# Kernel optimization log

Hardware: AMD Instinct MI355X
Metric: run time of the kernel (lower is better)

The kernel has to match this reference:

```python
import jax, jax.numpy as jnp
import numpy as np

B, IN, OUT, K, RES, WDIM = 8, 512, 512, 3, 64, 512
CONV_RC = 1.0 / np.sqrt(K * K * IN).astype(np.float32)   # gain*lrmul/sqrt(fan_in), gain=lrmul=1
DENSE_RC = 1.0 / np.sqrt(WDIM).astype(np.float32)
CONV_INIT_STD = float(CONV_RC)   # init_std = he_std / lrmul
DENSE_INIT_STD = float(DENSE_RC)


def setup_inputs() -> dict:
    key = jax.random.key(0)
    k1, k2, k3, k4 = jax.random.split(key, 4)
    return {
        "x": jax.random.normal(k1, (B, IN, RES, RES), jnp.float32),
        "y": jax.random.normal(k2, (B, WDIM), jnp.float32),
        "w": jax.random.normal(k3, (K, K, IN, OUT), jnp.float32) * CONV_INIT_STD,
        "w_mod": jax.random.normal(k4, (WDIM, IN), jnp.float32) * DENSE_INIT_STD,
        "b_mod": jnp.zeros((IN,), jnp.float32),
    }


def reference(x, y, w, w_mod, b_mod):
    # equalized-lr runtime scaling
    w_s = w * CONV_RC                                   # [K,K,IN,OUT]
    # style: s = dense(y) + bias + 1
    s = y @ (w_mod * DENSE_RC) + b_mod + 1.0            # [B,IN]
    # modulate per-sample weights
    ww = w_s[None] * s[:, None, None, :, None]          # [B,K,K,IN,OUT]
    # demodulate
    d = jax.lax.rsqrt(jnp.sum(jnp.square(ww), axis=(1, 2, 3)) + 1e-8)  # [B,OUT]
    ww = ww * d[:, None, None, None, :]
    # fused modconv: grouped conv with groups = B
    xr = x.reshape(1, B * IN, RES, RES)
    wk = jnp.transpose(ww, (1, 2, 3, 0, 4)).reshape(K, K, IN, B * OUT)
    out = jax.lax.conv_general_dilated(
        xr, wk, window_strides=(1, 1), padding="SAME",
        dimension_numbers=("NCHW", "HWIO", "NCHW"),
        feature_group_count=B)
    return out.reshape(B, OUT, RES, RES)
```

## Files before the change

kernel.cpp:

```cpp
#include <hip/hip_runtime.h>
#include <hip/hip_bf16.h>

typedef __bf16 bf16x8 __attribute__((ext_vector_type(8)));
typedef float f32x16 __attribute__((ext_vector_type(16)));
typedef unsigned short u16;
typedef u16 u16x8 __attribute__((ext_vector_type(8)));

#define DENSE_RC 0.0441941738f
#define CONV_RC  0.0147313913f

__device__ inline u16 f2bf(float v) {
  union { float f; unsigned u; } x; x.f = v;
  unsigned r = x.u + 0x7fffu + ((x.u >> 16) & 1u);
  return (u16)(r >> 16);
}

__device__ inline void gload16(const void* g, void* l) {
  __builtin_amdgcn_global_load_lds(
      (const __attribute__((address_space(1))) unsigned int*)g,
      (__attribute__((address_space(3))) unsigned int*)l, 16, 0, 0);
}

__global__ void style_k(const float* __restrict__ y, const float* __restrict__ wm,
                        const float* __restrict__ bm, float* __restrict__ s) {
  const int tid = threadIdx.x, lane = tid & 63, wv = tid >> 6;
  const int idx = blockIdx.x * 64 + lane;
  const int b = idx >> 9, i = idx & 511;
  const float* yb = y + b * 512;
  float acc = 0.f;
  const int j0 = wv * 128;
#pragma unroll 8
  for (int j = j0; j < j0 + 128; ++j) acc += yb[j] * wm[j * 512 + i];
  __shared__ float red[4][64];
  red[wv][lane] = acc;
  __syncthreads();
  if (wv == 0) {
    float a = red[0][lane] + red[1][lane] + red[2][lane] + red[3][lane];
    s[idx] = a * DENSE_RC + bm[i] + 1.0f;
  }
}

__global__ void wsq_k(const float* __restrict__ w, float* __restrict__ wsq) {
  const int idx = blockIdx.x * 256 + threadIdx.x;
  float a = 0.f;
#pragma unroll
  for (int t = 0; t < 9; ++t) { float v = w[(size_t)t * 262144 + idx]; a += v * v; }
  wsq[idx] = a;
}

__global__ void demod_k(const float* __restrict__ s, const float* __restrict__ wsq,
                        float* __restrict__ dmd) {
  const int tid = threadIdx.x, lane = tid & 63, wv = tid >> 6;
  const int idx = blockIdx.x * 64 + lane;
  const int b = idx >> 9, o = idx & 511;
  const float* sb = s + b * 512;
  float a = 0.f;
  const int i0 = wv * 128;
#pragma unroll 4
  for (int i = i0; i < i0 + 128; ++i) { float sv = sb[i]; a += sv * sv * wsq[i * 512 + o]; }
  __shared__ float red[4][64];
  red[wv][lane] = a;
  __syncthreads();
  if (wv == 0) {
    float t = red[0][lane] + red[1][lane] + red[2][lane] + red[3][lane];
    dmd[idx] = rsqrtf(t * (CONV_RC * CONV_RC) + 1e-8f);
  }
}

__global__ void modw_k(const float* __restrict__ w, const float* __restrict__ s,
                       const float* __restrict__ dmd, u16* __restrict__ wwb) {
  const int blk = blockIdx.x;
  const int ob = blk & 7, ib = (blk >> 3) & 15, t = blk >> 7;
  __shared__ float lw[32][65];
  const int tid = threadIdx.x;
#pragma unroll
  for (int k = 0; k < 8; ++k) {
    const int e = tid + k * 256;
    const int i = e >> 6, o = e & 63;
    lw[i][o] = w[(size_t)t * 262144 + (size_t)(ib * 32 + i) * 512 + ob * 64 + o];
  }
  __syncthreads();
  const int oo = tid >> 2, q = tid & 3;
  const int ii0 = q * 8;
  for (int b = 0; b < 8; ++b) {
    const float f = CONV_RC * dmd[b * 512 + ob * 64 + oo];
    u16x8 pk;
#pragma unroll
    for (int j = 0; j < 8; ++j)
      pk[j] = f2bf(lw[ii0 + j][oo] * s[b * 512 + ib * 32 + ii0 + j] * f);
    *(u16x8*)(wwb + ((size_t)(b * 9 + t) * 512 + ob * 64 + oo) * 512 + ib * 32 + ii0) = pk;
  }
}

__global__ void border_k(u16* __restrict__ xpad) {
  const int idx = blockIdx.x * 256 + threadIdx.x;
  const int chunk = idx & 63;
  const int p = (idx >> 6) % 260;
  const int b = idx / (260 * 64);
  int row, col;
  if (p < 66)       { row = 0;       col = p; }
  else if (p < 132) { row = 65;      col = p - 66; }
  else if (p < 196) { row = p - 131; col = 0; }
  else              { row = p - 195; col = 65; }
  u16x8 z = {0, 0, 0, 0, 0, 0, 0, 0};
  *(u16x8*)(xpad + ((size_t)(b * 66 + row) * 66 + col) * 512 + chunk * 8) = z;
}

__global__ void fill_k(const float* __restrict__ x, u16* __restrict__ xpad) {
  const int blk = blockIdx.x;
  const int ib = blk & 3, hh = (blk >> 2) & 63, b = blk >> 8;
  __shared__ float lx[128][65];
  const int tid = threadIdx.x;
#pragma unroll
  for (int k = 0; k < 2; ++k) {
    const int u = tid + k * 256;
    const int i = u >> 2, w0 = (u & 3) * 16;
    const float* src = x + (size_t)((b * 512 + ib * 128 + i) * 64 + hh) * 64 + w0;
    float tmp[16];
    ((float4*)tmp)[0] = ((const float4*)src)[0];
    ((float4*)tmp)[1] = ((const float4*)src)[1];
    ((float4*)tmp)[2] = ((const float4*)src)[2];
    ((float4*)tmp)[3] = ((const float4*)src)[3];
#pragma unroll
    for (int j = 0; j < 16; ++j) lx[i][w0 + j] = tmp[j];
  }
  __syncthreads();
  const int c = tid >> 2, q = tid & 3;
  const size_t base = ((size_t)(b * 66 + hh + 1) * 66 + (c + 1)) * 512 + ib * 128;
#pragma unroll
  for (int k = 0; k < 4; ++k) {
    const int irow = k * 32 + q * 8;
    u16x8 pk;
#pragma unroll
    for (int j = 0; j < 8; ++j) pk[j] = f2bf(lx[irow + j][c]);
    *(u16x8*)(xpad + base + irow) = pk;
  }
}

__global__ __launch_bounds__(256, 2) void conv_k(const u16* __restrict__ xpad,
                                                 const u16* __restrict__ wwb,
                                                 float* __restrict__ out) {
  __shared__ __align__(1024) char SM[79104];
  const int raw = (int)blockIdx.x;
  const int pt = raw >> 6, ot = (raw >> 3) & 7, b = raw & 7;
  const int tid = threadIdx.x;
  const int lane = tid & 63, wv = tid >> 6;
  const int h0 = pt * 8;

  const size_t xbase = (size_t)(b * 66 + h0) * (66 * 512);

  const u16* aw[9];
  const u16* ax[11];
#pragma unroll
  for (int r = 0; r < 9; ++r) {
    const int cc = tid + r * 256;
    const int lc = cc ^ ((cc >> 3) & 3);
    const int i8 = lc & 3, o = (lc >> 2) & 63, t = lc >> 8;
    aw[r] = wwb + ((size_t)(b * 9 + t) * 512 + ot * 64 + o) * 512 + i8 * 8;
  }
#pragma unroll
  for (int r = 0; r < 11; ++r) {
    const int c2 = tid + r * 256;
    const int lc = c2 ^ ((c2 >> 3) & 3);
    const int i8 = lc & 3, rc = lc >> 2;
    ax[r] = xpad + xbase + (size_t)rc * 512 + i8 * 8;
  }
  const bool extra = (tid < 80);

  const int pxl = lane & 31, i5 = lane >> 5;
  const int cbA = pxl * 4 + i5;
  const int AbO = (cbA ^ ((cbA >> 3) & 3)) * 16;
  int Boff[4][3];
#pragma unroll
  for (int rr = 0; rr < 4; ++rr)
#pragma unroll
    for (int tx = 0; tx < 3; ++tx) {
      const int m = (2 * wv + rr) * 66 + tx + pxl;
      const int ch = m * 4 + i5;
      Boff[rr][tx] = (ch ^ ((ch >> 3) & 3)) * 16;
    }

  f32x16 acc[2][2][2];
#pragma unroll
  for (int mi = 0; mi < 2; ++mi)
#pragma unroll
    for (int hf = 0; hf < 2; ++hf)
#pragma unroll
      for (int n = 0; n < 2; ++n)
#pragma unroll
        for (int e = 0; e < 16; ++e) acc[mi][hf][n][e] = 0.f;

#define LOADB(R, rr, tx) { \
    const int _o = Boff[rr][tx]; \
    R[0] = *(const bf16x8*)(SM + 36864 + _o); \
    R[1] = *(const bf16x8*)(SM + 36864 + (_o ^ 32)); \
    R[2] = *(const bf16x8*)(SM + 36864 + _o + 2048); \
    R[3] = *(const bf16x8*)(SM + 36864 + ((_o + 2048) ^ 32)); }
#define LOADA(af, t) { \
    const int _a = AbO + (t) * 4096; \
    af[0] = *(const bf16x8*)(SM + _a); \
    af[1] = *(const bf16x8*)(SM + (_a ^ 32)); \
    af[2] = *(const bf16x8*)(SM + _a + 2048); \
    af[3] = *(const bf16x8*)(SM + ((_a + 2048) ^ 32)); }
#define TAP(af, Blo, Bhi) \
    acc[0][0][0] = __builtin_amdgcn_mfma_f32_32x32x16_bf16(af[0], Blo[0], acc[0][0][0], 0, 0, 0); \
    acc[0][0][1] = __builtin_amdgcn_mfma_f32_32x32x16_bf16(af[0], Blo[2], acc[0][0][1], 0, 0, 0); \
    acc[0][1][0] = __builtin_amdgcn_mfma_f32_32x32x16_bf16(af[0], Bhi[0], acc[0][1][0], 0, 0, 0); \
    acc[0][1][1] = __builtin_amdgcn_mfma_f32_32x32x16_bf16(af[0], Bhi[2], acc[0][1][1], 0, 0, 0); \
    acc[1][0][0] = __builtin_amdgcn_mfma_f32_32x32x16_bf16(af[2], Blo[0], acc[1][0][0], 0, 0, 0); \
    acc[1][0][1] = __builtin_amdgcn_mfma_f32_32x32x16_bf16(af[2], Blo[2], acc[1][0][1], 0, 0, 0); \
    acc[1][1][0] = __builtin_amdgcn_mfma_f32_32x32x16_bf16(af[2], Bhi[0], acc[1][1][0], 0, 0, 0); \
    acc[1][1][1] = __builtin_amdgcn_mfma_f32_32x32x16_bf16(af[2], Bhi[2], acc[1][1][1], 0, 0, 0); \
    acc[0][0][0] = __builtin_amdgcn_mfma_f32_32x32x16_bf16(af[1], Blo[1], acc[0][0][0], 0, 0, 0); \
    acc[0][0][1] = __builtin_amdgcn_mfma_f32_32x32x16_bf16(af[1], Blo[3], acc[0][0][1], 0, 0, 0); \
    acc[0][1][0] = __builtin_amdgcn_mfma_f32_32x32x16_bf16(af[1], Bhi[1], acc[0][1][0], 0, 0, 0); \
    acc[0][1][1] = __builtin_amdgcn_mfma_f32_32x32x16_bf16(af[1], Bhi[3], acc[0][1][1], 0, 0, 0); \
    acc[1][0][0] = __builtin_amdgcn_mfma_f32_32x32x16_bf16(af[3], Blo[1], acc[1][0][0], 0, 0, 0); \
    acc[1][0][1] = __builtin_amdgcn_mfma_f32_32x32x16_bf16(af[3], Blo[3], acc[1][0][1], 0, 0, 0); \
    acc[1][1][0] = __builtin_amdgcn_mfma_f32_32x32x16_bf16(af[3], Bhi[1], acc[1][1][0], 0, 0, 0); \
    acc[1][1][1] = __builtin_amdgcn_mfma_f32_32x32x16_bf16(af[3], Bhi[3], acc[1][1][1], 0, 0, 0);

  for (int kb = 0; kb < 16; ++kb) {
#pragma unroll
    for (int r = 0; r < 9; ++r)
      gload16(aw[r], SM + (tid + r * 256) * 16);
#pragma unroll
    for (int r = 0; r < 10; ++r)
      gload16(ax[r], SM + 36864 + (tid + r * 256) * 16);
    if (extra) gload16(ax[10], SM + 36864 + (tid + 2560) * 16);
#pragma unroll
    for (int r = 0; r < 9; ++r) aw[r] += 32;
#pragma unroll
    for (int r = 0; r < 11; ++r) ax[r] += 32;
    asm volatile("s_waitcnt vmcnt(0)" ::: "memory");
    __syncthreads();

#pragma unroll
    for (int tx = 0; tx < 3; ++tx) {
      bf16x8 R0[4], R1[4], R2[4], R3[4], af0[4], af1[4], af2[4];
      LOADB(R0, 0, tx);
      LOADB(R1, 1, tx);
      LOADA(af0, tx);
      TAP(af0, R0, R1);
      LOADB(R2, 2, tx);
      LOADA(af1, 3 + tx);
      TAP(af1, R1, R2);
      LOADB(R3, 3, tx);
      LOADA(af2, 6 + tx);
      TAP(af2, R2, R3);
    }
    __syncthreads();
  }

  const int o4 = i5 * 4;
#pragma unroll
  for (int mi = 0; mi < 2; ++mi)
#pragma unroll
    for (int hf = 0; hf < 2; ++hf) {
      const int h = h0 + 2 * wv + hf;
#pragma unroll
      for (int n = 0; n < 2; ++n) {
        const int wc = n * 32 + pxl;
#pragma unroll
        for (int reg = 0; reg < 16; ++reg) {
          const int o = ot * 64 + mi * 32 + (reg & 3) + 8 * (reg >> 2) + o4;
          out[((size_t)(b * 512 + o) * 64 + h) * 64 + wc] = acc[mi][hf][n][reg];
        }
      }
    }
#undef LOADB
#undef LOADA
#undef TAP
}

extern "C" void kernel_launch(void* const* d_in, const int* in_sizes, int n_in,
                              void* d_out, int out_size, void* d_ws, size_t ws_size,
                              hipStream_t stream) {
  const float* x     = (const float*)d_in[0];
  const float* y     = (const float*)d_in[1];
  const float* w     = (const float*)d_in[2];
  const float* w_mod = (const float*)d_in[3];
  const float* b_mod = (const float*)d_in[4];
  float* out = (float*)d_out;

  char* ws = (char*)d_ws;
  float* s    = (float*)(ws);
  float* dmd  = (float*)(ws + 16384);
  float* wsq  = (float*)(ws + 32768);
  u16*   wwb  = (u16*)(ws + 32768 + 1048576);
  u16*   xpad = (u16*)(ws + 32768 + 1048576 + 37748736);

  style_k<<<64, 256, 0, stream>>>(y, w_mod, b_mod, s);
  wsq_k<<<1024, 256, 0, stream>>>(w, wsq);
  demod_k<<<64, 256, 0, stream>>>(s, wsq, dmd);
  modw_k<<<1152, 256, 0, stream>>>(w, s, dmd, wwb);
  border_k<<<520, 256, 0, stream>>>(xpad);
  fill_k<<<2048, 256, 0, stream>>>(x, xpad);
  conv_k<<<512, 256, 0, stream>>>(xpad, wwb, out);
}
```

Baseline: 174.0 us.

## Replace XOR-swizzled LDS layout with planar padded layout; widen modw tiles

The conv kernel's shared-memory staging drops the XOR swizzle and uses a planar layout: the i8 channel chunks are separated by fixed strides, and the input rows are padded (264-element rows, 4224-byte row stride). This makes the LDS address arithmetic for the A and B fragments simple constant offsets instead of a per-thread offset table, cutting register use and index computation. The global-to-LDS load addressing is rewritten to match, now using divisions by 264 and 66. Separately, the weight-modulation kernel processes 64 input channels per block and writes two 16-byte packs per thread, which halves the block count. The new layout risks LDS bank conflicts that the swizzle previously avoided.

Measured after the change: 186.5 us. 1.07x slower.

```diff
diff --git a/kernel.cpp b/kernel.cpp
--- a/kernel.cpp
+++ b/kernel.cpp
@@ -70,25 +70,30 @@
 __global__ void modw_k(const float* __restrict__ w, const float* __restrict__ s,
                        const float* __restrict__ dmd, u16* __restrict__ wwb) {
   const int blk = blockIdx.x;
-  const int ob = blk & 7, ib = (blk >> 3) & 15, t = blk >> 7;
-  __shared__ float lw[32][65];
+  const int ob = blk & 7, ib = (blk >> 3) & 7, t = blk >> 6;
+  __shared__ float lw[64][65];
   const int tid = threadIdx.x;
 #pragma unroll
-  for (int k = 0; k < 8; ++k) {
+  for (int k = 0; k < 16; ++k) {
     const int e = tid + k * 256;
     const int i = e >> 6, o = e & 63;
-    lw[i][o] = w[(size_t)t * 262144 + (size_t)(ib * 32 + i) * 512 + ob * 64 + o];
+    lw[i][o] = w[(size_t)t * 262144 + (size_t)(ib * 64 + i) * 512 + ob * 64 + o];
   }
   __syncthreads();
   const int oo = tid >> 2, q = tid & 3;
-  const int ii0 = q * 8;
+  const int ii0 = q * 16;
   for (int b = 0; b < 8; ++b) {
     const float f = CONV_RC * dmd[b * 512 + ob * 64 + oo];
-    u16x8 pk;
-#pragma unroll
-    for (int j = 0; j < 8; ++j)
-      pk[j] = f2bf(lw[ii0 + j][oo] * s[b * 512 + ib * 32 + ii0 + j] * f);
-    *(u16x8*)(wwb + ((size_t)(b * 9 + t) * 512 + ob * 64 + oo) * 512 + ib * 32 + ii0) = pk;
+    const float* sb = s + b * 512 + ib * 64;
+    u16x8 pk0, pk1;
+#pragma unroll
+    for (int j = 0; j < 8; ++j) {
+      pk0[j] = f2bf(lw[ii0 + j][oo] * sb[ii0 + j] * f);
+      pk1[j] = f2bf(lw[ii0 + 8 + j][oo] * sb[ii0 + 8 + j] * f);
+    }
+    u16* dst = wwb + ((size_t)(b * 9 + t) * 512 + ob * 64 + oo) * 512 + ib * 64 + ii0;
+    *(u16x8*)dst = pk0;
+    *(u16x8*)(dst + 8) = pk1;
   }
 }
 
@@ -154,31 +159,20 @@
 #pragma unroll
   for (int r = 0; r < 9; ++r) {
     const int cc = tid + r * 256;
-    const int lc = cc ^ ((cc >> 3) & 3);
-    const int i8 = lc & 3, o = (lc >> 2) & 63, t = lc >> 8;
+    const int t = cc >> 8, rem = cc & 255, i8 = rem >> 6, o = rem & 63;
     aw[r] = wwb + ((size_t)(b * 9 + t) * 512 + ot * 64 + o) * 512 + i8 * 8;
   }
 #pragma unroll
   for (int r = 0; r < 11; ++r) {
     const int c2 = tid + r * 256;
-    const int lc = c2 ^ ((c2 >> 3) & 3);
-    const int i8 = lc & 3, rc = lc >> 2;
-    ax[r] = xpad + xbase + (size_t)rc * 512 + i8 * 8;
+    const int row = c2 / 264, rem2 = c2 % 264, i8 = rem2 / 66, col = rem2 % 66;
+    ax[r] = xpad + xbase + (size_t)(row * 66 + col) * 512 + i8 * 8;
   }
   const bool extra = (tid < 80);
 
   const int pxl = lane & 31, i5 = lane >> 5;
-  const int cbA = pxl * 4 + i5;
-  const int AbO = (cbA ^ ((cbA >> 3) & 3)) * 16;
-  int Boff[4][3];
-#pragma unroll
-  for (int rr = 0; rr < 4; ++rr)
-#pragma unroll
-    for (int tx = 0; tx < 3; ++tx) {
-      const int m = (2 * wv + rr) * 66 + tx + pxl;
-      const int ch = m * 4 + i5;
-      Boff[rr][tx] = (ch ^ ((ch >> 3) & 3)) * 16;
-    }
+  const int AbO = i5 * 1024 + pxl * 16;
+  const int BbO = i5 * 1056 + pxl * 16;
 
   f32x16 acc[2][2][2];
 #pragma unroll
@@ -191,17 +185,17 @@
         for (int e = 0; e < 16; ++e) acc[mi][hf][n][e] = 0.f;
 
 #define LOADB(R, rr, tx) { \
-    const int _o = Boff[rr][tx]; \
-    R[0] = *(const bf16x8*)(SM + 36864 + _o); \
-    R[1] = *(const bf16x8*)(SM + 36864 + (_o ^ 32)); \
-    R[2] = *(const bf16x8*)(SM + 36864 + _o + 2048); \
-    R[3] = *(const bf16x8*)(SM + 36864 + ((_o + 2048) ^ 32)); }
+    const char* _p = SM + 36864 + BbO + (2 * wv + (rr)) * 4224 + (tx) * 16; \
+    R[0] = *(const bf16x8*)(_p); \
+    R[1] = *(const bf16x8*)(_p + 2112); \
+    R[2] = *(const bf16x8*)(_p + 512); \
+    R[3] = *(const bf16x8*)(_p + 2624); }
 #define LOADA(af, t) { \
-    const int _a = AbO + (t) * 4096; \
-    af[0] = *(const bf16x8*)(SM + _a); \
-    af[1] = *(const bf16x8*)(SM + (_a ^ 32)); \
-    af[2] = *(const bf16x8*)(SM + _a + 2048); \
-    af[3] = *(const bf16x8*)(SM + ((_a + 2048) ^ 32)); }
+    const char* _p = SM + AbO + (t) * 4096; \
+    af[0] = *(const bf16x8*)(_p); \
+    af[1] = *(const bf16x8*)(_p + 2048); \
+    af[2] = *(const bf16x8*)(_p + 512); \
+    af[3] = *(const bf16x8*)(_p + 2560); }
 #define TAP(af, Blo, Bhi) \
     acc[0][0][0] = __builtin_amdgcn_mfma_f32_32x32x16_bf16(af[0], Blo[0], acc[0][0][0], 0, 0, 0); \
     acc[0][0][1] = __builtin_amdgcn_mfma_f32_32x32x16_bf16(af[0], Blo[2], acc[0][0][1], 0, 0, 0); \
@@ -293,7 +287,7 @@
   style_k<<<64, 256, 0, stream>>>(y, w_mod, b_mod, s);
   wsq_k<<<1024, 256, 0, stream>>>(w, wsq);
   demod_k<<<64, 256, 0, stream>>>(s, wsq, dmd);
-  modw_k<<<1152, 256, 0, stream>>>(w, s, dmd, wwb);
+  modw_k<<<576, 256, 0, stream>>>(w, s, dmd, wwb);
   border_k<<<520, 256, 0, stream>>>(xpad);
   fill_k<<<2048, 256, 0, stream>>>(x, xpad);
   conv_k<<<512, 256, 0, stream>>>(xpad, wwb, out);
```
